# Kernel tuning notes

Hardware: AMD Instinct MI355X
Metric: run time of the kernel (lower is better)

The kernel has to match this reference:

```python
import jax, jax.numpy as jnp
import numpy as np

BLOCK = 8  # block_size from init_kwargs


def _zigzag(n):
    # Same traversal as zigzag_indices() in the original module.
    idx = np.zeros(n * n, dtype=np.int64)
    i = j = 0
    for k in range(n * n):
        idx[k] = i * n + j
        if (i + j) % 2 == 0:  # moving up-right
            if j == n - 1:
                i += 1
            elif i == 0:
                j += 1
            else:
                i -= 1
                j += 1
        else:  # moving down-left
            if i == n - 1:
                j += 1
            elif j == 0:
                i += 1
            else:
                i += 1
                j -= 1
    return idx


def _dct_basis(N):
    # dct() with norm=None is DCT-II: V[k] = 2 * sum_n x[n] cos(pi*(2n+1)k/(2N))
    k = np.arange(N)[:, None].astype(np.float64)
    nn = np.arange(N)[None, :].astype(np.float64)
    return (2.0 * np.cos(np.pi * (2.0 * nn + 1.0) * k / (2.0 * N))).astype(np.float32)


def setup_inputs() -> dict:
    key = jax.random.key(0)
    img = jax.random.normal(key, (16, 3, 512, 512), dtype=jnp.float32)
    return {"img": img}


def reference(img):
    B = BLOCK
    bs, c, h, w = img.shape
    hb, wb = h // B, w // B
    n = hb * wb
    m = hb  # square grid: m = sqrt(n)

    # split_blocks: unfold(2,B,B).unfold(3,B,B) -> [bs,c,hb,wb,B,B] -> [bs,n,c,B,B]
    blocks = (
        img.reshape(bs, c, hb, B, wb, B)
        .transpose(0, 2, 4, 1, 3, 5)
        .reshape(bs, n, c, B, B)
    )

    # dct_2d with norm=None as separable matmuls against the DCT-II basis
    C = jnp.asarray(_dct_basis(B))  # [B, B] basis, C[k, x]
    z = jnp.einsum("uh,vw,bnchw->bncuv", C, C, blocks)  # [bs,n,c,B,B]

    # frequencyFeat: zigzag-reorder the B*B coeffs, then tile blocks into an m x m map
    zz = jnp.asarray(_zigzag(B))
    flat = z.reshape(bs, n, c, B * B)[..., zz]  # [bs,n,c,B*B]
    feat = (
        flat.reshape(bs, m, m, c, B * B)
        .transpose(0, 3, 4, 1, 2)
        .reshape(bs, c * B * B, m, m)
    )
    return feat
```

## Files before the change

kernel.cpp:

```cpp
#include <hip/hip_runtime.h>


__device__ __constant__ int INVZZ[64] = {
     0,  1,  5,  6, 14, 15, 27, 28,
     2,  4,  7, 13, 16, 26, 29, 42,
     3,  8, 12, 17, 25, 30, 41, 43,
     9, 11, 18, 24, 31, 40, 44, 53,
    10, 19, 23, 32, 39, 45, 52, 54,
    20, 22, 33, 38, 46, 51, 55, 60,
    21, 34, 37, 47, 50, 56, 59, 61,
    35, 36, 48, 49, 57, 58, 62, 63
};

__global__ __launch_bounds__(256) void dct2d_zigzag_kernel(
    const float* __restrict__ img, float* __restrict__ out)
{
    constexpr float c1 = 1.9615705608064609f;
    constexpr float c2 = 1.8477590650225735f;
    constexpr float c3 = 1.6629392246050905f;
    constexpr float c4 = 1.4142135623730951f;
    constexpr float c5 = 1.1111404660392044f;
    constexpr float c6 = 0.7653668647301796f;
    constexpr float c7 = 0.3901806440322565f;
    const float C[8][8] = {
        { 2.f,  2.f,  2.f,  2.f,  2.f,  2.f,  2.f,  2.f},
        { c1,   c3,   c5,   c7,  -c7,  -c5,  -c3,  -c1},
        { c2,   c6,  -c6,  -c2,  -c2,  -c6,   c6,   c2},
        { c3,  -c7,  -c1,  -c5,   c5,   c1,   c7,  -c3},
        { c4,  -c4,  -c4,   c4,   c4,  -c4,  -c4,   c4},
        { c5,  -c1,   c7,   c3,  -c3,  -c7,   c1,  -c5},
        { c6,  -c2,   c2,  -c6,  -c6,   c2,  -c2,   c6},
        { c7,  -c5,   c3,  -c1,   c1,  -c3,   c5,  -c7},
    };

    const int tid = blockIdx.x * 256 + threadIdx.x;
    const int bj = tid & 63;
    const int bi = (tid >> 6) & 63;
    const int bc = tid >> 12;

    const float* __restrict__ src =
        img + (size_t)bc * 262144 + (size_t)bi * 8 * 512 + (size_t)bj * 8;

    float X[8][8];
#pragma unroll
    for (int r = 0; r < 8; ++r) {
        const float4 lo = *reinterpret_cast<const float4*>(src + r * 512);
        const float4 hi = *reinterpret_cast<const float4*>(src + r * 512 + 4);
        X[r][0] = lo.x; X[r][1] = lo.y; X[r][2] = lo.z; X[r][3] = lo.w;
        X[r][4] = hi.x; X[r][5] = hi.y; X[r][6] = hi.z; X[r][7] = hi.w;
    }

    float* __restrict__ dst =
        out + (size_t)bc * 262144 + (size_t)bi * 64 + (size_t)bj;

#pragma unroll
    for (int u = 0; u < 8; ++u) {
        float t[8];
#pragma unroll
        for (int x = 0; x < 8; ++x) {
            float s = C[u][0] * X[0][x];
#pragma unroll
            for (int y = 1; y < 8; ++y) s += C[u][y] * X[y][x];
            t[x] = s;
        }
#pragma unroll
        for (int v = 0; v < 8; ++v) {
            float s = t[0] * C[v][0];
#pragma unroll
            for (int x = 1; x < 8; ++x) s += t[x] * C[v][x];
            dst[(size_t)INVZZ[u * 8 + v] * 4096] = s;
        }
    }
}

extern "C" void kernel_launch(void* const* d_in, const int* in_sizes, int n_in,
                              void* d_out, int out_size, void* d_ws, size_t ws_size,
                              hipStream_t stream)
{
    const float* img = (const float*)d_in[0];
    float* out = (float*)d_out;
    dct2d_zigzag_kernel<<<768, 256, 0, stream>>>(img, out);
}
```

Measured before the change: 98.68 us.

## Use butterfly-factored separable 8-point DCT with compile-time zigzag store indices

Replaces the direct 8x8 matrix products with an even/odd butterfly factorization of the 8-point DCT-II, first applied along rows as each row is loaded and then along columns. This cuts the FMA count per block. The zigzag output positions are now hardcoded at compile time instead of read from a constant-memory table. Summation order changes, so floating-point rounding differs slightly, and the kernel is likely memory-bound, which may limit the benefit.

Measured after the change: 96.26 us. 2.5% less time.

```diff
diff --git a/kernel.cpp b/kernel.cpp
--- a/kernel.cpp
+++ b/kernel.cpp
@@ -1,76 +1,79 @@
 #include <hip/hip_runtime.h>
 
 
-__device__ __constant__ int INVZZ[64] = {
-     0,  1,  5,  6, 14, 15, 27, 28,
-     2,  4,  7, 13, 16, 26, 29, 42,
-     3,  8, 12, 17, 25, 30, 41, 43,
-     9, 11, 18, 24, 31, 40, 44, 53,
-    10, 19, 23, 32, 39, 45, 52, 54,
-    20, 22, 33, 38, 46, 51, 55, 60,
-    21, 34, 37, 47, 50, 56, 59, 61,
-    35, 36, 48, 49, 57, 58, 62, 63
-};
+#define K1 1.9615705608064609f
+#define K2 1.8477590650225735f
+#define K3 1.6629392246050905f
+#define K4 1.4142135623730951f
+#define K5 1.1111404660392044f
+#define K6 0.7653668647301796f
+#define K7 0.3901806440322565f
+
+#define DCT8(x0,x1,x2,x3,x4,x5,x6,x7, y0,y1,y2,y3,y4,y5,y6,y7) do {        \
+    float s0=(x0)+(x7), s1=(x1)+(x6), s2=(x2)+(x5), s3=(x3)+(x4);          \
+    float d0=(x0)-(x7), d1=(x1)-(x6), d2=(x2)-(x5), d3=(x3)-(x4);          \
+    float e0=s0+s3, e1=s1+s2, o0=s0-s3, o1=s1-s2;                          \
+    y0 = 2.0f*(e0+e1);                                                     \
+    y4 = K4*(e0-e1);                                                       \
+    y2 = K2*o0 + K6*o1;                                                    \
+    y6 = K6*o0 - K2*o1;                                                    \
+    y1 = K1*d0 + K3*d1 + K5*d2 + K7*d3;                                    \
+    y3 = K3*d0 - K7*d1 - K1*d2 - K5*d3;                                    \
+    y5 = K5*d0 - K1*d1 + K7*d2 + K3*d3;                                    \
+    y7 = K7*d0 - K5*d1 + K3*d2 - K1*d3;                                    \
+} while (0)
+
+#define ROWDCT(r) do {                                                     \
+    const float4 lo = *reinterpret_cast<const float4*>(src + (r)*512);     \
+    const float4 hi = *reinterpret_cast<const float4*>(src + (r)*512 + 4); \
+    DCT8(lo.x,lo.y,lo.z,lo.w,hi.x,hi.y,hi.z,hi.w,                          \
+         t##r##0,t##r##1,t##r##2,t##r##3,t##r##4,t##r##5,t##r##6,t##r##7); \
+} while (0)
+
+#define COLSTORE(v, p0,p1,p2,p3,p4,p5,p6,p7) do {                          \
+    float z0,z1,z2,z3,z4,z5,z6,z7;                                         \
+    DCT8(t0##v,t1##v,t2##v,t3##v,t4##v,t5##v,t6##v,t7##v,                  \
+         z0,z1,z2,z3,z4,z5,z6,z7);                                         \
+    dst[(size_t)(p0)*4096] = z0;  dst[(size_t)(p1)*4096] = z1;             \
+    dst[(size_t)(p2)*4096] = z2;  dst[(size_t)(p3)*4096] = z3;             \
+    dst[(size_t)(p4)*4096] = z4;  dst[(size_t)(p5)*4096] = z5;             \
+    dst[(size_t)(p6)*4096] = z6;  dst[(size_t)(p7)*4096] = z7;             \
+} while (0)
 
 __global__ __launch_bounds__(256) void dct2d_zigzag_kernel(
     const float* __restrict__ img, float* __restrict__ out)
 {
-    constexpr float c1 = 1.9615705608064609f;
-    constexpr float c2 = 1.8477590650225735f;
-    constexpr float c3 = 1.6629392246050905f;
-    constexpr float c4 = 1.4142135623730951f;
-    constexpr float c5 = 1.1111404660392044f;
-    constexpr float c6 = 0.7653668647301796f;
-    constexpr float c7 = 0.3901806440322565f;
-    const float C[8][8] = {
-        { 2.f,  2.f,  2.f,  2.f,  2.f,  2.f,  2.f,  2.f},
-        { c1,   c3,   c5,   c7,  -c7,  -c5,  -c3,  -c1},
-        { c2,   c6,  -c6,  -c2,  -c2,  -c6,   c6,   c2},
-        { c3,  -c7,  -c1,  -c5,   c5,   c1,   c7,  -c3},
-        { c4,  -c4,  -c4,   c4,   c4,  -c4,  -c4,   c4},
-        { c5,  -c1,   c7,   c3,  -c3,  -c7,   c1,  -c5},
-        { c6,  -c2,   c2,  -c6,  -c6,   c2,  -c2,   c6},
-        { c7,  -c5,   c3,  -c1,   c1,  -c3,   c5,  -c7},
-    };
-
     const int tid = blockIdx.x * 256 + threadIdx.x;
     const int bj = tid & 63;
     const int bi = (tid >> 6) & 63;
     const int bc = tid >> 12;
 
     const float* __restrict__ src =
-        img + (size_t)bc * 262144 + (size_t)bi * 8 * 512 + (size_t)bj * 8;
-
-    float X[8][8];
-#pragma unroll
-    for (int r = 0; r < 8; ++r) {
-        const float4 lo = *reinterpret_cast<const float4*>(src + r * 512);
-        const float4 hi = *reinterpret_cast<const float4*>(src + r * 512 + 4);
-        X[r][0] = lo.x; X[r][1] = lo.y; X[r][2] = lo.z; X[r][3] = lo.w;
-        X[r][4] = hi.x; X[r][5] = hi.y; X[r][6] = hi.z; X[r][7] = hi.w;
-    }
+        img + (size_t)bc * 262144 + (size_t)bi * 4096 + (size_t)bj * 8;
 
     float* __restrict__ dst =
         out + (size_t)bc * 262144 + (size_t)bi * 64 + (size_t)bj;
 
-#pragma unroll
-    for (int u = 0; u < 8; ++u) {
-        float t[8];
-#pragma unroll
-        for (int x = 0; x < 8; ++x) {
-            float s = C[u][0] * X[0][x];
-#pragma unroll
-            for (int y = 1; y < 8; ++y) s += C[u][y] * X[y][x];
-            t[x] = s;
-        }
-#pragma unroll
-        for (int v = 0; v < 8; ++v) {
-            float s = t[0] * C[v][0];
-#pragma unroll
-            for (int x = 1; x < 8; ++x) s += t[x] * C[v][x];
-            dst[(size_t)INVZZ[u * 8 + v] * 4096] = s;
-        }
-    }
+    float t00,t01,t02,t03,t04,t05,t06,t07;
+    float t10,t11,t12,t13,t14,t15,t16,t17;
+    float t20,t21,t22,t23,t24,t25,t26,t27;
+    float t30,t31,t32,t33,t34,t35,t36,t37;
+    float t40,t41,t42,t43,t44,t45,t46,t47;
+    float t50,t51,t52,t53,t54,t55,t56,t57;
+    float t60,t61,t62,t63,t64,t65,t66,t67;
+    float t70,t71,t72,t73,t74,t75,t76,t77;
+
+    ROWDCT(0); ROWDCT(1); ROWDCT(2); ROWDCT(3);
+    ROWDCT(4); ROWDCT(5); ROWDCT(6); ROWDCT(7);
+
+    COLSTORE(0,  0,  2,  3,  9, 10, 20, 21, 35);
+    COLSTORE(1,  1,  4,  8, 11, 19, 22, 34, 36);
+    COLSTORE(2,  5,  7, 12, 18, 23, 33, 37, 48);
+    COLSTORE(3,  6, 13, 17, 24, 32, 38, 47, 49);
+    COLSTORE(4, 14, 16, 25, 31, 39, 46, 50, 57);
+    COLSTORE(5, 15, 26, 30, 40, 45, 51, 56, 58);
+    COLSTORE(6, 27, 29, 41, 44, 52, 55, 59, 62);
+    COLSTORE(7, 28, 42, 43, 53, 54, 60, 61, 63);
 }
 
 extern "C" void kernel_launch(void* const* d_in, const int* in_sizes, int n_in,
```
